# Kernel tuning notes

Hardware: AMD Instinct MI355X
Metric: run time of the kernel (lower is better)

Reference implementation:

```python
import jax, jax.numpy as jnp
import numpy as np

IN_DIM = 4096
UNITS = 4096
BATCH = 4096
SIGMA_INIT = 0.5


def _scale_noise(key, size):
    x = jax.random.normal(key, (size,), dtype=jnp.float32)
    return jnp.sign(x) * jnp.sqrt(jnp.abs(x))


def setup_inputs() -> dict:
    key = jax.random.key(0)
    kx, kwmu, kbmu, kein, keout = jax.random.split(key, 5)
    bound = 1.0 / np.sqrt(IN_DIM)
    x = jax.random.normal(kx, (BATCH, IN_DIM), dtype=jnp.float32)
    w_mu = jax.random.uniform(kwmu, (IN_DIM, UNITS), minval=-bound, maxval=bound, dtype=jnp.float32)
    w_sigma = jnp.full((IN_DIM, UNITS), SIGMA_INIT * bound, dtype=jnp.float32)
    b_mu = jax.random.uniform(kbmu, (UNITS,), minval=-bound, maxval=bound, dtype=jnp.float32)
    b_sigma = jnp.full((UNITS,), SIGMA_INIT * bound, dtype=jnp.float32)
    eps_in = _scale_noise(kein, IN_DIM)
    eps_out = _scale_noise(keout, UNITS)
    return {"x": x, "w_mu": w_mu, "w_sigma": w_sigma, "b_mu": b_mu,
            "b_sigma": b_sigma, "eps_in": eps_in, "eps_out": eps_out}


def reference(x, w_mu, w_sigma, b_mu, b_sigma, eps_in, eps_out):
    # training-mode NoisyDense: w = w_mu + w_sigma * outer(eps_in, eps_out)
    eps_w = eps_in[:, None] * eps_out[None, :]        # [IN_DIM, UNITS]
    w = w_mu + w_sigma * eps_w
    b = b_mu + b_sigma * eps_out
    out = jnp.matmul(x, w) + b                         # [BATCH, UNITS]
    return jax.nn.relu(out)
```

## Files before the change

kernel.cpp:

```cpp
#include <hip/hip_runtime.h>
#include <hip/hip_bf16.h>
#include <stdint.h>

#define M_DIM 4096
#define K_DIM 4096
#define N_DIM 4096

typedef __bf16 bf16_t;
typedef __bf16  bf16x8 __attribute__((ext_vector_type(8)));
typedef float   f32x4  __attribute__((ext_vector_type(4)));
typedef float   floatx4 __attribute__((ext_vector_type(4)));

__device__ __forceinline__ void gload_lds16(const bf16_t* g, bf16_t* l) {
    __builtin_amdgcn_global_load_lds(
        (const __attribute__((address_space(1))) void*)(uintptr_t)g,
        (__attribute__((address_space(3))) void*)(uintptr_t)(unsigned)(uintptr_t)l,
        16, 0, 0);
}

__global__ __launch_bounds__(256) void convert_x(const float* __restrict__ x,
                                                 bf16_t* __restrict__ xb) {
    size_t idx = (size_t)blockIdx.x * blockDim.x + threadIdx.x;
    const floatx4* x4 = (const floatx4*)x;
    floatx4 a = x4[idx * 2];
    floatx4 b = x4[idx * 2 + 1];
    bf16x8 o;
    o[0] = (bf16_t)a[0]; o[1] = (bf16_t)a[1]; o[2] = (bf16_t)a[2]; o[3] = (bf16_t)a[3];
    o[4] = (bf16_t)b[0]; o[5] = (bf16_t)b[1]; o[6] = (bf16_t)b[2]; o[7] = (bf16_t)b[3];
    *(bf16x8*)&xb[idx * 8] = o;
}

__global__ __launch_bounds__(256) void build_wt(const float* __restrict__ w_mu,
                                                const float* __restrict__ w_sigma,
                                                const float* __restrict__ eps_in,
                                                const float* __restrict__ eps_out,
                                                bf16_t* __restrict__ wt) {
    __shared__ float tile[64][65];
    int bk = blockIdx.x & 63;
    int bn = blockIdx.x >> 6;
    int k0 = bk * 64, n0 = bn * 64;
    int t = threadIdx.x;
    int c = t & 63;
    float eo = eps_out[n0 + c];
#pragma unroll
    for (int p = 0; p < 16; ++p) {
        int r = p * 4 + (t >> 6);
        int k = k0 + r;
        float ei = eps_in[k];
        size_t off = (size_t)k * N_DIM + n0 + c;
        tile[r][c] = w_mu[off] + w_sigma[off] * (ei * eo);
    }
    __syncthreads();
#pragma unroll
    for (int p = 0; p < 8; ++p) {
        int rn = p * 8 + (t >> 5);
        int ck = (t & 31) * 2;
        bf16_t v0 = (bf16_t)tile[ck][rn];
        bf16_t v1 = (bf16_t)tile[ck + 1][rn];
        union { bf16_t b[2]; unsigned u; } u2;
        u2.b[0] = v0; u2.b[1] = v1;
        *(unsigned*)&wt[(size_t)(n0 + rn) * K_DIM + k0 + ck] = u2.u;
    }
}

#define BM 256
#define BN 256
#define BK 64
#define NT (K_DIM / BK)

__device__ __forceinline__ void stage_half(bf16_t* lds, const bf16_t* g, int kcol0, int t) {
#pragma unroll
    for (int p = 0; p < 2; ++p) {
        int chunk = p * 512 + t;
        int row = chunk >> 3;
        int c16 = chunk & 7;
        gload_lds16(g + (size_t)row * K_DIM + kcol0 + ((c16 ^ (row & 7)) << 3),
                    lds + row * BK + (c16 << 3));
    }
}

__device__ __forceinline__ bf16x8 lds_frag(const bf16_t* base, int row, int kcol) {
    int c16 = kcol >> 3;
    return *(const bf16x8*)(base + row * BK + (((c16 ^ (row & 7)) << 3)));
}

#define BAR()  asm volatile("s_barrier" ::: "memory")

__global__ __launch_bounds__(512, 2) void gemm8p(
    const bf16_t* __restrict__ A,
    const bf16_t* __restrict__ Bt,
    const float* __restrict__ b_mu,
    const float* __restrict__ b_sigma,
    const float* __restrict__ eps_out,
    float* __restrict__ C) {

    __shared__ __align__(16) bf16_t As[2][BM * BK];
    __shared__ __align__(16) bf16_t Bs[2][BN * BK];

    int bid = blockIdx.x;
    int swz = (bid & 7) * (gridDim.x >> 3) + (bid >> 3);
    int tm = swz & 15, tn = swz >> 4;
    size_t bm = (size_t)tm * BM, bn = (size_t)tn * BN;

    int t = threadIdx.x;
    int lane = t & 63;
    int wave = t >> 6;
    int wr = wave >> 2, wc = wave & 3;
    int l15 = lane & 15;
    int kseg = (lane >> 4) << 3;

    const bf16_t* Ab = A  + bm * (size_t)K_DIM;
    const bf16_t* Bb = Bt + bn * (size_t)K_DIM;

    f32x4 zero = {0.f, 0.f, 0.f, 0.f};
    f32x4 acc[8][4];
#pragma unroll
    for (int i = 0; i < 8; ++i)
#pragma unroll
        for (int j = 0; j < 4; ++j) acc[i][j] = zero;

    stage_half(&As[0][0],            Ab,                        0, t);
    stage_half(&As[0][128 * BK],     Ab + (size_t)128 * K_DIM,  0, t);
    stage_half(&Bs[0][0],            Bb,                        0, t);
    stage_half(&Bs[0][128 * BK],     Bb + (size_t)128 * K_DIM,  0, t);
    stage_half(&As[1][0],            Ab,                        BK, t);
    asm volatile("s_waitcnt vmcnt(2)" ::: "memory");
    BAR();

    for (int kt = 0; kt < NT; ++kt) {
        const int cur = kt & 1, nxt = cur ^ 1;
        const bf16_t* As_c = &As[cur][0];
        const bf16_t* Bs_c = &Bs[cur][0];
        const int kb1 = (kt + 1) * BK;
        const int kb2 = (kt + 2) * BK;
        const bool st1 = (kt + 1 < NT);
        bf16x8 af[4][2], bq0[2][2], bq1[2][2];

#pragma unroll
        for (int mi = 0; mi < 4; ++mi)
#pragma unroll
            for (int kk = 0; kk < 2; ++kk)
                af[mi][kk] = lds_frag(As_c, wr * 128 + mi * 16 + l15, kk * 32 + kseg);
#pragma unroll
        for (int ni = 0; ni < 2; ++ni)
#pragma unroll
            for (int kk = 0; kk < 2; ++kk)
                bq0[ni][kk] = lds_frag(Bs_c, wc * 64 + ni * 16 + l15, kk * 32 + kseg);
        if (st1) stage_half(&As[nxt][128 * BK], Ab + (size_t)128 * K_DIM, kb1, t);
        BAR();
        __builtin_amdgcn_s_setprio(1);
#pragma unroll
        for (int mi = 0; mi < 4; ++mi)
#pragma unroll
            for (int ni = 0; ni < 2; ++ni)
#pragma unroll
                for (int kk = 0; kk < 2; ++kk)
                    acc[mi][ni] = __builtin_amdgcn_mfma_f32_16x16x32_bf16(
                        af[mi][kk], bq0[ni][kk], acc[mi][ni], 0, 0, 0);
        __builtin_amdgcn_s_setprio(0);
        BAR();

#pragma unroll
        for (int ni = 0; ni < 2; ++ni)
#pragma unroll
            for (int kk = 0; kk < 2; ++kk)
                bq1[ni][kk] = lds_frag(Bs_c, wc * 64 + 32 + ni * 16 + l15, kk * 32 + kseg);
        if (st1) stage_half(&Bs[nxt][0], Bb, kb1, t);
        BAR();
        __builtin_amdgcn_s_setprio(1);
#pragma unroll
        for (int mi = 0; mi < 4; ++mi)
#pragma unroll
            for (int ni = 0; ni < 2; ++ni)
#pragma unroll
                for (int kk = 0; kk < 2; ++kk)
                    acc[mi][2 + ni] = __builtin_amdgcn_mfma_f32_16x16x32_bf16(
                        af[mi][kk], bq1[ni][kk], acc[mi][2 + ni], 0, 0, 0);
        __builtin_amdgcn_s_setprio(0);
        BAR();

#pragma unroll
        for (int mi = 0; mi < 4; ++mi)
#pragma unroll
            for (int kk = 0; kk < 2; ++kk)
                af[mi][kk] = lds_frag(As_c, wr * 128 + 64 + mi * 16 + l15, kk * 32 + kseg);
        if (st1) stage_half(&Bs[nxt][128 * BK], Bb + (size_t)128 * K_DIM, kb1, t);
        BAR();
        __builtin_amdgcn_s_setprio(1);
#pragma unroll
        for (int mi = 0; mi < 4; ++mi)
#pragma unroll
            for (int ni = 0; ni < 2; ++ni)
#pragma unroll
                for (int kk = 0; kk < 2; ++kk)
                    acc[4 + mi][2 + ni] = __builtin_amdgcn_mfma_f32_16x16x32_bf16(
                        af[mi][kk], bq1[ni][kk], acc[4 + mi][2 + ni], 0, 0, 0);
        __builtin_amdgcn_s_setprio(0);
        BAR();

        if (kt + 2 < NT) stage_half(&As[cur][0], Ab, kb2, t);
        BAR();
        __builtin_amdgcn_s_setprio(1);
#pragma unroll
        for (int mi = 0; mi < 4; ++mi)
#pragma unroll
            for (int ni = 0; ni < 2; ++ni)
#pragma unroll
                for (int kk = 0; kk < 2; ++kk)
                    acc[4 + mi][ni] = __builtin_amdgcn_mfma_f32_16x16x32_bf16(
                        af[mi][kk], bq0[ni][kk], acc[4 + mi][ni], 0, 0, 0);
        __builtin_amdgcn_s_setprio(0);
        if (kt < NT - 2) {
            asm volatile("s_waitcnt vmcnt(2)" ::: "memory");
        } else if (kt == NT - 2) {
            asm volatile("s_waitcnt vmcnt(0)" ::: "memory");
        }
        BAR();
    }

    int col0 = l15;
    int row0 = (lane >> 4) * 4;
#pragma unroll
    for (int qn = 0; qn < 2; ++qn)
#pragma unroll
        for (int ni = 0; ni < 2; ++ni) {
            int n = (int)bn + wc * 64 + qn * 32 + ni * 16 + col0;
            float bias = b_mu[n] + b_sigma[n] * eps_out[n];
#pragma unroll
            for (int qm = 0; qm < 2; ++qm)
#pragma unroll
                for (int mi = 0; mi < 4; ++mi) {
                    int m = (int)bm + wr * 128 + qm * 64 + mi * 16 + row0;
                    f32x4 v = acc[qm * 4 + mi][qn * 2 + ni];
#pragma unroll
                    for (int r = 0; r < 4; ++r) {
                        float o = v[r] + bias;
                        C[(size_t)(m + r) * N_DIM + n] = o > 0.f ? o : 0.f;
                    }
                }
        }
}

extern "C" void kernel_launch(void* const* d_in, const int* in_sizes, int n_in,
                              void* d_out, int out_size, void* d_ws, size_t ws_size,
                              hipStream_t stream) {
    const float* x       = (const float*)d_in[0];
    const float* w_mu    = (const float*)d_in[1];
    const float* w_sigma = (const float*)d_in[2];
    const float* b_mu    = (const float*)d_in[3];
    const float* b_sigma = (const float*)d_in[4];
    const float* eps_in  = (const float*)d_in[5];
    const float* eps_out = (const float*)d_in[6];
    float* out = (float*)d_out;

    bf16_t* xb = (bf16_t*)d_ws;
    bf16_t* wt = (bf16_t*)((char*)d_ws + (size_t)M_DIM * K_DIM * 2);

    convert_x<<<(M_DIM * K_DIM) / (8 * 256), 256, 0, stream>>>(x, xb);
    build_wt<<<64 * 64, 256, 0, stream>>>(w_mu, w_sigma, eps_in, eps_out, wt);
    gemm8p<<<(M_DIM / BM) * (N_DIM / BN), 512, 0, stream>>>(
        xb, wt, b_mu, b_sigma, eps_out, out);
}
```

Measured before the change: 170.7 us.

## Restructure GEMM k-loop into single-tile-ahead prefetch with three barrier phases

Replaces the staggered half-tile prefetch, which loaded part of A two tiles ahead, with a plain double buffer. All of the next B tile and half of the next A tile are issued in the first phase. The remaining A quarters are issued in the second phase, and vmcnt waits are placed just before the data is read. The last two MFMA phases are merged, which removes one barrier pair per k-iteration. The trade-off is larger load bursts per phase and a different latency-hiding window for the late A quarters.

```diff
diff --git a/kernel.cpp b/kernel.cpp
--- a/kernel.cpp
+++ b/kernel.cpp
@@ -68,15 +68,11 @@
 #define BK 64
 #define NT (K_DIM / BK)
 
-__device__ __forceinline__ void stage_half(bf16_t* lds, const bf16_t* g, int kcol0, int t) {
-#pragma unroll
-    for (int p = 0; p < 2; ++p) {
-        int chunk = p * 512 + t;
-        int row = chunk >> 3;
-        int c16 = chunk & 7;
-        gload_lds16(g + (size_t)row * K_DIM + kcol0 + ((c16 ^ (row & 7)) << 3),
-                    lds + row * BK + (c16 << 3));
-    }
+__device__ __forceinline__ void stage_q(bf16_t* lds, const bf16_t* g, int kcol0, int t) {
+    int row = t >> 3;
+    int c16 = t & 7;
+    gload_lds16(g + (size_t)row * K_DIM + kcol0 + ((c16 ^ (row & 7)) << 3),
+                lds + row * BK + (c16 << 3));
 }
 
 __device__ __forceinline__ bf16x8 lds_frag(const bf16_t* base, int row, int kcol) {
@@ -119,22 +115,23 @@
 #pragma unroll
         for (int j = 0; j < 4; ++j) acc[i][j] = zero;
 
-    stage_half(&As[0][0],            Ab,                        0, t);
-    stage_half(&As[0][128 * BK],     Ab + (size_t)128 * K_DIM,  0, t);
-    stage_half(&Bs[0][0],            Bb,                        0, t);
-    stage_half(&Bs[0][128 * BK],     Bb + (size_t)128 * K_DIM,  0, t);
-    stage_half(&As[1][0],            Ab,                        BK, t);
-    asm volatile("s_waitcnt vmcnt(2)" ::: "memory");
+#pragma unroll
+    for (int q = 0; q < 4; ++q) {
+        stage_q(&As[0][q * 64 * BK], Ab + (size_t)(q * 64) * K_DIM, 0, t);
+        stage_q(&Bs[0][q * 64 * BK], Bb + (size_t)(q * 64) * K_DIM, 0, t);
+    }
+    asm volatile("s_waitcnt vmcnt(0)" ::: "memory");
     BAR();
 
     for (int kt = 0; kt < NT; ++kt) {
         const int cur = kt & 1, nxt = cur ^ 1;
         const bf16_t* As_c = &As[cur][0];
         const bf16_t* Bs_c = &Bs[cur][0];
+        bf16_t* As_n = &As[nxt][0];
+        bf16_t* Bs_n = &Bs[nxt][0];
         const int kb1 = (kt + 1) * BK;
-        const int kb2 = (kt + 2) * BK;
-        const bool st1 = (kt + 1 < NT);
-        bf16x8 af[4][2], bq0[2][2], bq1[2][2];
+        const bool st = (kt + 1 < NT);
+        bf16x8 af[4][2], b0[2][2], b1[2][2];
 
 #pragma unroll
         for (int mi = 0; mi < 4; ++mi)
@@ -145,8 +142,15 @@
         for (int ni = 0; ni < 2; ++ni)
 #pragma unroll
             for (int kk = 0; kk < 2; ++kk)
-                bq0[ni][kk] = lds_frag(Bs_c, wc * 64 + ni * 16 + l15, kk * 32 + kseg);
-        if (st1) stage_half(&As[nxt][128 * BK], Ab + (size_t)128 * K_DIM, kb1, t);
+                b0[ni][kk] = lds_frag(Bs_c, wc * 64 + ni * 16 + l15, kk * 32 + kseg);
+        if (st) {
+            stage_q(Bs_n,                Bb,                        kb1, t);
+            stage_q(Bs_n + 64 * BK,      Bb + (size_t)64 * K_DIM,   kb1, t);
+            stage_q(Bs_n + 128 * BK,     Bb + (size_t)128 * K_DIM,  kb1, t);
+            stage_q(Bs_n + 192 * BK,     Bb + (size_t)192 * K_DIM,  kb1, t);
+            stage_q(As_n,                Ab,                        kb1, t);
+            stage_q(As_n + 128 * BK,     Ab + (size_t)128 * K_DIM,  kb1, t);
+        }
         BAR();
         __builtin_amdgcn_s_setprio(1);
 #pragma unroll
@@ -156,7 +160,7 @@
 #pragma unroll
                 for (int kk = 0; kk < 2; ++kk)
                     acc[mi][ni] = __builtin_amdgcn_mfma_f32_16x16x32_bf16(
-                        af[mi][kk], bq0[ni][kk], acc[mi][ni], 0, 0, 0);
+                        af[mi][kk], b0[ni][kk], acc[mi][ni], 0, 0, 0);
         __builtin_amdgcn_s_setprio(0);
         BAR();
 
@@ -164,8 +168,11 @@
         for (int ni = 0; ni < 2; ++ni)
 #pragma unroll
             for (int kk = 0; kk < 2; ++kk)
-                bq1[ni][kk] = lds_frag(Bs_c, wc * 64 + 32 + ni * 16 + l15, kk * 32 + kseg);
-        if (st1) stage_half(&Bs[nxt][0], Bb, kb1, t);
+                b1[ni][kk] = lds_frag(Bs_c, wc * 64 + 32 + ni * 16 + l15, kk * 32 + kseg);
+        if (st) {
+            stage_q(As_n + 64 * BK,  Ab + (size_t)64 * K_DIM,  kb1, t);
+            stage_q(As_n + 192 * BK, Ab + (size_t)192 * K_DIM, kb1, t);
+        }
         BAR();
         __builtin_amdgcn_s_setprio(1);
 #pragma unroll
@@ -175,8 +182,13 @@
 #pragma unroll
                 for (int kk = 0; kk < 2; ++kk)
                     acc[mi][2 + ni] = __builtin_amdgcn_mfma_f32_16x16x32_bf16(
-                        af[mi][kk], bq1[ni][kk], acc[mi][2 + ni], 0, 0, 0);
+                        af[mi][kk], b1[ni][kk], acc[mi][2 + ni], 0, 0, 0);
         __builtin_amdgcn_s_setprio(0);
+        if (kt == NT - 1) {
+            asm volatile("s_waitcnt vmcnt(0)" ::: "memory");
+        } else {
+            asm volatile("s_waitcnt vmcnt(8)" ::: "memory");
+        }
         BAR();
 
 #pragma unroll
@@ -184,7 +196,6 @@
 #pragma unroll
             for (int kk = 0; kk < 2; ++kk)
                 af[mi][kk] = lds_frag(As_c, wr * 128 + 64 + mi * 16 + l15, kk * 32 + kseg);
-        if (st1) stage_half(&Bs[nxt][128 * BK], Bb + (size_t)128 * K_DIM, kb1, t);
         BAR();
         __builtin_amdgcn_s_setprio(1);
 #pragma unroll
@@ -194,27 +205,17 @@
 #pragma unroll
                 for (int kk = 0; kk < 2; ++kk)
                     acc[4 + mi][2 + ni] = __builtin_amdgcn_mfma_f32_16x16x32_bf16(
-                        af[mi][kk], bq1[ni][kk], acc[4 + mi][2 + ni], 0, 0, 0);
+                        af[mi][kk], b1[ni][kk], acc[4 + mi][2 + ni], 0, 0, 0);
+#pragma unroll
+        for (int mi = 0; mi < 4; ++mi)
+#pragma unroll
+            for (int ni = 0; ni < 2; ++ni)
+#pragma unroll
+                for (int kk = 0; kk < 2; ++kk)
+                    acc[4 + mi][ni] = __builtin_amdgcn_mfma_f32_16x16x32_bf16(
+                        af[mi][kk], b0[ni][kk], acc[4 + mi][ni], 0, 0, 0);
         __builtin_amdgcn_s_setprio(0);
-        BAR();
-
-        if (kt + 2 < NT) stage_half(&As[cur][0], Ab, kb2, t);
-        BAR();
-        __builtin_amdgcn_s_setprio(1);
-#pragma unroll
-        for (int mi = 0; mi < 4; ++mi)
-#pragma unroll
-            for (int ni = 0; ni < 2; ++ni)
-#pragma unroll
-                for (int kk = 0; kk < 2; ++kk)
-                    acc[4 + mi][ni] = __builtin_amdgcn_mfma_f32_16x16x32_bf16(
-                        af[mi][kk], bq0[ni][kk], acc[4 + mi][ni], 0, 0, 0);
-        __builtin_amdgcn_s_setprio(0);
-        if (kt < NT - 2) {
-            asm volatile("s_waitcnt vmcnt(2)" ::: "memory");
-        } else if (kt == NT - 2) {
-            asm volatile("s_waitcnt vmcnt(0)" ::: "memory");
-        }
+        asm volatile("s_waitcnt vmcnt(2)" ::: "memory");
         BAR();
     }
 
```

After: 175.3 us. +2.7%, slower.

## Restructure GEMM pipeline with per-quadrant staging and cross-tile fragment prefetch

Applied to the files above, without the earlier changes.

Reorganizes the double-buffered bf16 GEMM main loop so global-to-LDS staging is split by the row sets each wave quadrant consumes (interleaved 64-row and 32-row groups) instead of contiguous halves. Fragments for the next K tile (A upper rows and B first columns) are loaded from the next buffer during the last two MFMA phases of the current tile, with register ping-pong between two B fragment sets and an unrolled-by-two loop. The aim is to hide LDS read latency at tile boundaries and shorten the wait before each MFMA block. The buffer-reuse ordering and vmcnt accounting are now more intricate, which risks stalls or register pressure at two waves per SIMD.

```diff
diff --git a/kernel.cpp b/kernel.cpp
--- a/kernel.cpp
+++ b/kernel.cpp
@@ -68,23 +68,102 @@
 #define BK 64
 #define NT (K_DIM / BK)
 
-__device__ __forceinline__ void stage_half(bf16_t* lds, const bf16_t* g, int kcol0, int t) {
+__device__ __forceinline__ void stage_Aset(bf16_t* lds, const bf16_t* g, int kcol0, int t, int off) {
 #pragma unroll
     for (int p = 0; p < 2; ++p) {
         int chunk = p * 512 + t;
-        int row = chunk >> 3;
+        int r = chunk >> 3;
+        int row = ((r >> 6) << 7) + (r & 63) + off;
         int c16 = chunk & 7;
         gload_lds16(g + (size_t)row * K_DIM + kcol0 + ((c16 ^ (row & 7)) << 3),
                     lds + row * BK + (c16 << 3));
     }
 }
 
+__device__ __forceinline__ void stage_Bset(bf16_t* lds, const bf16_t* g, int kcol0, int t, int off) {
+#pragma unroll
+    for (int p = 0; p < 2; ++p) {
+        int chunk = p * 512 + t;
+        int r = chunk >> 3;
+        int row = ((r >> 5) << 6) + (r & 31) + off;
+        int c16 = chunk & 7;
+        gload_lds16(g + (size_t)row * K_DIM + kcol0 + ((c16 ^ (row & 7)) << 3),
+                    lds + row * BK + (c16 << 3));
+    }
+}
+
 __device__ __forceinline__ bf16x8 lds_frag(const bf16_t* base, int row, int kcol) {
     int c16 = kcol >> 3;
     return *(const bf16x8*)(base + row * BK + (((c16 ^ (row & 7)) << 3)));
 }
 
-#define BAR()  asm volatile("s_barrier" ::: "memory")
+#define BAR() asm volatile("s_barrier" ::: "memory")
+#define VM2() asm volatile("s_waitcnt vmcnt(2)" ::: "memory")
+#define VM0() asm volatile("s_waitcnt vmcnt(0)" ::: "memory")
+
+#define MFMA16(QM, QN, AARR, BARR)                                                 \
+    _Pragma("unroll") for (int mi = 0; mi < 4; ++mi)                               \
+    _Pragma("unroll") for (int ni = 0; ni < 2; ++ni)                               \
+    _Pragma("unroll") for (int kk = 0; kk < 2; ++kk)                               \
+        acc[(QM) * 4 + mi][(QN) * 2 + ni] = __builtin_amdgcn_mfma_f32_16x16x32_bf16( \
+            AARR[mi][kk], BARR[ni][kk], acc[(QM) * 4 + mi][(QN) * 2 + ni], 0, 0, 0);
+
+#define TILE_BODY(KT, AS_C, AS_N, BS_C, BS_N, B0A, B1A)                            \
+{                                                                                  \
+    const int kb1_ = ((KT) + 1) * BK;                                              \
+    const bool st_ = ((KT) + 1 < NT);                                              \
+                             \
+    _Pragma("unroll") for (int ni = 0; ni < 2; ++ni)                               \
+    _Pragma("unroll") for (int kk = 0; kk < 2; ++kk)                               \
+        B1A[ni][kk] = lds_frag(BS_C, wc * 64 + 32 + ni * 16 + l15, kk * 32 + kseg);\
+    if (st_) stage_Aset(AS_N, Ab, kb1_, t, 0);                                     \
+    BAR();                                                                         \
+    __builtin_amdgcn_s_setprio(1);                                                 \
+    MFMA16(0, 0, aU, B0A)                                                          \
+    __builtin_amdgcn_s_setprio(0);                                                 \
+    if ((KT) == NT - 1) { VM0(); } else { VM2(); }                                 \
+    BAR();                                                                         \
+                             \
+    _Pragma("unroll") for (int mi = 0; mi < 4; ++mi)                               \
+    _Pragma("unroll") for (int kk = 0; kk < 2; ++kk)                               \
+        aV[mi][kk] = lds_frag(AS_C, wr * 128 + 64 + mi * 16 + l15, kk * 32 + kseg);\
+    if (st_) stage_Bset(BS_N, Bb, kb1_, t, 0);                                     \
+    BAR();                                                                         \
+    __builtin_amdgcn_s_setprio(1);                                                 \
+    MFMA16(0, 1, aU, B1A)                                                          \
+    __builtin_amdgcn_s_setprio(0);                                                 \
+    VM2();                                                                         \
+    BAR();                                                                         \
+              \
+    if (st_) {                                                                     \
+        _Pragma("unroll") for (int mi = 0; mi < 2; ++mi)                           \
+        _Pragma("unroll") for (int kk = 0; kk < 2; ++kk)                           \
+            aU[mi][kk] = lds_frag(AS_N, wr * 128 + mi * 16 + l15, kk * 32 + kseg); \
+        stage_Bset(BS_N, Bb, kb1_, t, 32);                                         \
+    }                                                                              \
+    BAR();                                                                         \
+    __builtin_amdgcn_s_setprio(1);                                                 \
+    MFMA16(1, 1, aV, B1A)                                                          \
+    __builtin_amdgcn_s_setprio(0);                                                 \
+    VM2();                                                                         \
+    BAR();                                                                         \
+     \
+    if (st_) {                                                                     \
+        _Pragma("unroll") for (int mi = 2; mi < 4; ++mi)                           \
+        _Pragma("unroll") for (int kk = 0; kk < 2; ++kk)                           \
+            aU[mi][kk] = lds_frag(AS_N, wr * 128 + mi * 16 + l15, kk * 32 + kseg); \
+        _Pragma("unroll") for (int ni = 0; ni < 2; ++ni)                           \
+        _Pragma("unroll") for (int kk = 0; kk < 2; ++kk)                           \
+            B1A[ni][kk] = lds_frag(BS_N, wc * 64 + ni * 16 + l15, kk * 32 + kseg); \
+        stage_Aset(AS_N, Ab, kb1_, t, 64);                                         \
+    }                                                                              \
+    BAR();                                                                         \
+    __builtin_amdgcn_s_setprio(1);                                                 \
+    MFMA16(1, 0, aV, B0A)                                                          \
+    __builtin_amdgcn_s_setprio(0);                                                 \
+    VM2();                                                                         \
+    BAR();                                                                         \
+}
 
 __global__ __launch_bounds__(512, 2) void gemm8p(
     const bf16_t* __restrict__ A,
@@ -119,103 +198,28 @@
 #pragma unroll
         for (int j = 0; j < 4; ++j) acc[i][j] = zero;
 
-    stage_half(&As[0][0],            Ab,                        0, t);
-    stage_half(&As[0][128 * BK],     Ab + (size_t)128 * K_DIM,  0, t);
-    stage_half(&Bs[0][0],            Bb,                        0, t);
-    stage_half(&Bs[0][128 * BK],     Bb + (size_t)128 * K_DIM,  0, t);
-    stage_half(&As[1][0],            Ab,                        BK, t);
-    asm volatile("s_waitcnt vmcnt(2)" ::: "memory");
+    bf16x8 aU[4][2], aV[4][2], bP[2][2], bQ[2][2];
+
+    stage_Aset(&As[0][0], Ab, 0, t, 0);
+    stage_Aset(&As[0][0], Ab, 0, t, 64);
+    stage_Bset(&Bs[0][0], Bb, 0, t, 0);
+    stage_Bset(&Bs[0][0], Bb, 0, t, 32);
+    VM0();
     BAR();
-
-    for (int kt = 0; kt < NT; ++kt) {
-        const int cur = kt & 1, nxt = cur ^ 1;
-        const bf16_t* As_c = &As[cur][0];
-        const bf16_t* Bs_c = &Bs[cur][0];
-        const int kb1 = (kt + 1) * BK;
-        const int kb2 = (kt + 2) * BK;
-        const bool st1 = (kt + 1 < NT);
-        bf16x8 af[4][2], bq0[2][2], bq1[2][2];
-
-#pragma unroll
-        for (int mi = 0; mi < 4; ++mi)
-#pragma unroll
-            for (int kk = 0; kk < 2; ++kk)
-                af[mi][kk] = lds_frag(As_c, wr * 128 + mi * 16 + l15, kk * 32 + kseg);
-#pragma unroll
-        for (int ni = 0; ni < 2; ++ni)
-#pragma unroll
-            for (int kk = 0; kk < 2; ++kk)
-                bq0[ni][kk] = lds_frag(Bs_c, wc * 64 + ni * 16 + l15, kk * 32 + kseg);
-        if (st1) stage_half(&As[nxt][128 * BK], Ab + (size_t)128 * K_DIM, kb1, t);
-        BAR();
-        __builtin_amdgcn_s_setprio(1);
-#pragma unroll
-        for (int mi = 0; mi < 4; ++mi)
-#pragma unroll
-            for (int ni = 0; ni < 2; ++ni)
-#pragma unroll
-                for (int kk = 0; kk < 2; ++kk)
-                    acc[mi][ni] = __builtin_amdgcn_mfma_f32_16x16x32_bf16(
-                        af[mi][kk], bq0[ni][kk], acc[mi][ni], 0, 0, 0);
-        __builtin_amdgcn_s_setprio(0);
-        BAR();
-
-#pragma unroll
-        for (int ni = 0; ni < 2; ++ni)
-#pragma unroll
-            for (int kk = 0; kk < 2; ++kk)
-                bq1[ni][kk] = lds_frag(Bs_c, wc * 64 + 32 + ni * 16 + l15, kk * 32 + kseg);
-        if (st1) stage_half(&Bs[nxt][0], Bb, kb1, t);
-        BAR();
-        __builtin_amdgcn_s_setprio(1);
-#pragma unroll
-        for (int mi = 0; mi < 4; ++mi)
-#pragma unroll
-            for (int ni = 0; ni < 2; ++ni)
-#pragma unroll
-                for (int kk = 0; kk < 2; ++kk)
-                    acc[mi][2 + ni] = __builtin_amdgcn_mfma_f32_16x16x32_bf16(
-                        af[mi][kk], bq1[ni][kk], acc[mi][2 + ni], 0, 0, 0);
-        __builtin_amdgcn_s_setprio(0);
-        BAR();
-
-#pragma unroll
-        for (int mi = 0; mi < 4; ++mi)
-#pragma unroll
-            for (int kk = 0; kk < 2; ++kk)
-                af[mi][kk] = lds_frag(As_c, wr * 128 + 64 + mi * 16 + l15, kk * 32 + kseg);
-        if (st1) stage_half(&Bs[nxt][128 * BK], Bb + (size_t)128 * K_DIM, kb1, t);
-        BAR();
-        __builtin_amdgcn_s_setprio(1);
-#pragma unroll
-        for (int mi = 0; mi < 4; ++mi)
-#pragma unroll
-            for (int ni = 0; ni < 2; ++ni)
-#pragma unroll
-                for (int kk = 0; kk < 2; ++kk)
-                    acc[4 + mi][2 + ni] = __builtin_amdgcn_mfma_f32_16x16x32_bf16(
-                        af[mi][kk], bq1[ni][kk], acc[4 + mi][2 + ni], 0, 0, 0);
-        __builtin_amdgcn_s_setprio(0);
-        BAR();
-
-        if (kt + 2 < NT) stage_half(&As[cur][0], Ab, kb2, t);
-        BAR();
-        __builtin_amdgcn_s_setprio(1);
-#pragma unroll
-        for (int mi = 0; mi < 4; ++mi)
-#pragma unroll
-            for (int ni = 0; ni < 2; ++ni)
-#pragma unroll
-                for (int kk = 0; kk < 2; ++kk)
-                    acc[4 + mi][ni] = __builtin_amdgcn_mfma_f32_16x16x32_bf16(
-                        af[mi][kk], bq0[ni][kk], acc[4 + mi][ni], 0, 0, 0);
-        __builtin_amdgcn_s_setprio(0);
-        if (kt < NT - 2) {
-            asm volatile("s_waitcnt vmcnt(2)" ::: "memory");
-        } else if (kt == NT - 2) {
-            asm volatile("s_waitcnt vmcnt(0)" ::: "memory");
-        }
-        BAR();
+#pragma unroll
+    for (int mi = 0; mi < 4; ++mi)
+#pragma unroll
+        for (int kk = 0; kk < 2; ++kk)
+            aU[mi][kk] = lds_frag(&As[0][0], wr * 128 + mi * 16 + l15, kk * 32 + kseg);
+#pragma unroll
+    for (int ni = 0; ni < 2; ++ni)
+#pragma unroll
+        for (int kk = 0; kk < 2; ++kk)
+            bP[ni][kk] = lds_frag(&Bs[0][0], wc * 64 + ni * 16 + l15, kk * 32 + kseg);
+
+    for (int kt2 = 0; kt2 < NT; kt2 += 2) {
+        TILE_BODY(kt2,     (&As[0][0]), (&As[1][0]), (&Bs[0][0]), (&Bs[1][0]), bP, bQ)
+        TILE_BODY(kt2 + 1, (&As[1][0]), (&As[0][0]), (&Bs[1][0]), (&Bs[0][0]), bQ, bP)
     }
 
     int col0 = l15;
```

New measurement: 269.1 us (median of 2 runs). +57.7%, slower.
